# Kernel optimization log

Hardware: AMD Instinct MI355X
Metric: run time of the kernel (lower is better)

Reference implementation:

```python
import jax, jax.numpy as jnp
import numpy as np

CUTOFF = 5.0
BOX = 15.0
SPECIES = [1, 6, 8]
N_NODES = 10000
N_EDGES = 200000
ETAS = [0.01, 0.05, 0.1]
ZETAS = [1.0, 2.0, 4.0, 8.0]
LAMBDAS = [-1.0, 1.0]


def _cartesian_params():
    # matches torch.cartesian_prod(etas, zetas, lambdas): etas outermost
    e, zt, lb = np.meshgrid(np.float32(ETAS), np.float32(ZETAS), np.float32(LAMBDAS), indexing='ij')
    return e.ravel(), zt.ravel(), lb.ravel()  # each [24]


def _build_triplets(rng):
    # edges: edge_index[0]=j (source), edge_index[1]=i (target)
    j = rng.integers(0, N_NODES, N_EDGES)
    i = rng.integers(0, N_NODES, N_EDGES)
    edge_shift = rng.integers(-1, 2, (N_EDGES, 3)).astype(np.float32)
    # CSR of adj_t (row=i, col=j): for edge e, triplet partners k are cols of row j[e]
    order = np.argsort(i, kind='stable')
    cols = j[order]
    cnt = np.bincount(i, minlength=N_NODES)
    rowptr = np.concatenate([[0], np.cumsum(cnt)])
    num_trip = cnt[j]
    T = int(num_trip.sum())
    e_of_t = np.repeat(np.arange(N_EDGES), num_trip)
    starts = np.repeat(np.cumsum(num_trip) - num_trip, num_trip)
    local = np.arange(T) - starts
    idx_k = cols[rowptr[j[e_of_t]] + local]
    idx_i = i[e_of_t]
    idx_j = j[e_of_t]
    shift_t = edge_shift[e_of_t]
    m = idx_i != idx_k
    return idx_i[m], idx_j[m], idx_k[m], shift_t[m]


def setup_inputs() -> dict:
    rng = np.random.default_rng(0)
    pos = rng.uniform(0.0, BOX, (N_NODES, 3)).astype(np.float32)
    cell = (np.eye(3, dtype=np.float32) * BOX)[None]  # [1,3,3]
    z = np.asarray(SPECIES, dtype=np.int64)[rng.integers(0, 3, N_NODES)]
    batch = np.zeros(N_NODES, dtype=np.int64)
    idx_i, idx_j, idx_k, edge_shift_i = _build_triplets(rng)
    etas, zetas, lambdas = _cartesian_params()
    return {
        'pos': jnp.asarray(pos), 'cell': jnp.asarray(cell),
        'z': jnp.asarray(z), 'batch': jnp.asarray(batch),
        'idx_i': jnp.asarray(idx_i), 'idx_j': jnp.asarray(idx_j), 'idx_k': jnp.asarray(idx_k),
        'edge_shift_i': jnp.asarray(edge_shift_i),
        'etas': jnp.asarray(etas), 'zetas': jnp.asarray(zetas), 'lambdas': jnp.asarray(lambdas),
    }


def _cutoff_fn(r):
    return 0.5 * (jnp.cos(jnp.pi * r / CUTOFF) + 1.0) * (r < CUTOFF).astype(r.dtype)


def reference(pos, cell, z, batch, idx_i, idx_j, idx_k, edge_shift_i, etas, zetas, lambdas):
    n_nodes = pos.shape[0]
    pos_i = pos[idx_i]                       # [T,3]
    cell_t = cell[batch[idx_i]]              # [T,3,3]
    shift = jnp.einsum('ni,nij->nj', edge_shift_i, cell_t)
    vec_ij = pos[idx_j] - pos_i + shift
    vec_ik = pos[idx_k] - pos_i + shift
    r_ij = jnp.linalg.norm(vec_ij, axis=-1)
    r_ik = jnp.linalg.norm(vec_ik, axis=-1)
    r_jk = jnp.linalg.norm(vec_ik - vec_ij, axis=-1)
    cos_ijk = jnp.sum(vec_ij * vec_ik, axis=-1) / (r_ij * r_ik + 1e-12)

    # [P,T] angular descriptor; base (1 + lambda*cos) >= 0 since lambda = +/-1
    G4 = (jnp.power(2.0, 1.0 - zetas)[:, None]
          * jnp.power(1.0 + lambdas[:, None] * cos_ijk[None, :], zetas[:, None])
          * jnp.exp(-etas[:, None] * (r_ij**2 + r_ik**2 + r_jk**2)[None, :] / CUTOFF**2)
          * (_cutoff_fn(r_ij) * _cutoff_fn(r_ik) * _cutoff_fn(r_jk))[None, :])

    zj = z[idx_j]
    zk = z[idx_k]
    outs = []
    for sp in SPECIES:
        mask = ((zj == sp) & (zk == sp)).astype(G4.dtype)
        outs.append(jax.ops.segment_sum((G4 * mask).T, idx_i, num_segments=n_nodes).T / 2)
    pairs = [(SPECIES[a], SPECIES[b]) for a in range(len(SPECIES)) for b in range(a + 1, len(SPECIES))]
    for sp_j, sp_k in pairs:
        mask = (((zj == sp_j) & (zk == sp_k)) | ((zj == sp_k) & (zk == sp_j))).astype(G4.dtype)
        outs.append(jax.ops.segment_sum((G4 * mask).T, idx_i, num_segments=n_nodes).T / 2)
    return jnp.concatenate(outs, axis=0)  # [6*P, N]
```

## Files before the change

kernel.cpp:

```cpp
#include <hip/hip_runtime.h>
#include <math.h>

#define CUTOFF_R  5.0f
#define CUT2      25.0f
#define INV_CUT2  (1.0f / 25.0f)
#define PI_OVER_CUT (3.14159265358979323846f / CUTOFF_R)
#define NPARAM 24
#define TPT 4

__device__ __noinline__ void rare_accumulate(
    int i, int j, int k,
    float vjx, float vjy, float vjz,
    float vkx, float vky, float vkz,
    float r2ij, float r2ik, float r2jk,
    const int* __restrict__ z,
    const float* __restrict__ etas,
    float* __restrict__ out, int N)
{
    float rij = sqrtf(r2ij);
    float rik = sqrtf(r2ik);
    float rjk = sqrtf(r2jk);

    float fc = 0.125f * (cosf(PI_OVER_CUT * rij) + 1.0f)
                      * (cosf(PI_OVER_CUT * rik) + 1.0f)
                      * (cosf(PI_OVER_CUT * rjk) + 1.0f);

    float cos_ijk = (vjx * vkx + vjy * vky + vjz * vkz) / (rij * rik + 1e-12f);
    float ssum = (r2ij + r2ik + r2jk) * INV_CUT2;

    int zj = z[j], zk = z[k];
    int a = (zj == 1) ? 0 : ((zj == 6) ? 1 : 2);
    int c = (zk == 1) ? 0 : ((zk == 6) ? 1 : 2);
    int ch = (a == c) ? a : (2 + a + c);

    float* obase = out + (size_t)ch * NPARAM * N + i;
    float fch = 0.5f * fc;

    float bm = 1.0f - cos_ijk;
    float bp = 1.0f + cos_ijk;
    float pw[4][2];
    pw[0][0] = bm;                 pw[0][1] = bp;
    pw[1][0] = bm * bm;            pw[1][1] = bp * bp;
    pw[2][0] = pw[1][0]*pw[1][0];  pw[2][1] = pw[1][1]*pw[1][1];
    pw[3][0] = pw[2][0]*pw[2][0];  pw[3][1] = pw[2][1]*pw[2][1];
    const float coef[4] = {1.0f, 0.5f, 0.125f, 0.0078125f};

    #pragma unroll
    for (int e = 0; e < 3; ++e) {
        float ee = expf(-etas[e * 8] * ssum) * fch;
        #pragma unroll
        for (int zi = 0; zi < 4; ++zi) {
            float cz = coef[zi] * ee;
            atomicAdd(obase + (size_t)(e * 8 + zi * 2 + 0) * N, cz * pw[zi][0]);
            atomicAdd(obase + (size_t)(e * 8 + zi * 2 + 1) * N, cz * pw[zi][1]);
        }
    }
}

__global__ __launch_bounds__(256) void g4_kernel(
    const float* __restrict__ pos,
    const float* __restrict__ cell,
    const int*   __restrict__ z,
    const int*   __restrict__ batch,
    const int*   __restrict__ idx_i,
    const int*   __restrict__ idx_j,
    const int*   __restrict__ idx_k,
    const float* __restrict__ shift,
    const float* __restrict__ etas,
    float* __restrict__ out,
    int T, int N)
{
    int tid = blockIdx.x * blockDim.x + threadIdx.x;
    int base = tid * TPT;
    if (base >= T) return;

    if (base + TPT <= T) {
        int4 vi = *reinterpret_cast<const int4*>(idx_i + base);
        int4 vj = *reinterpret_cast<const int4*>(idx_j + base);
        int4 vk = *reinterpret_cast<const int4*>(idx_k + base);
        int ii[TPT] = {vi.x, vi.y, vi.z, vi.w};
        int jj[TPT] = {vj.x, vj.y, vj.z, vj.w};
        int kk[TPT] = {vk.x, vk.y, vk.z, vk.w};
        float sf[12];
        {
            const float4* sp = reinterpret_cast<const float4*>(shift + 3 * base);
            float4 a = sp[0], b = sp[1], c = sp[2];
            sf[0]=a.x; sf[1]=a.y; sf[2]=a.z;  sf[3]=a.w;
            sf[4]=b.x; sf[5]=b.y; sf[6]=b.z;  sf[7]=b.w;
            sf[8]=c.x; sf[9]=c.y; sf[10]=c.z; sf[11]=c.w;
        }

        float vjxa[TPT], vjya[TPT], vjza[TPT];
        float vkxa[TPT], vkya[TPT], vkza[TPT];
        float r2ija[TPT], r2ika[TPT], r2jka[TPT];
        unsigned mask = 0;

        #pragma unroll
        for (int m = 0; m < TPT; ++m) {
            int i = ii[m], j = jj[m], k = kk[m];
            int b = batch[i];
            const float* C = cell + 9 * b;
            float s0 = sf[3*m], s1 = sf[3*m+1], s2 = sf[3*m+2];
            float shx = s0 * C[0] + s1 * C[3] + s2 * C[6];
            float shy = s0 * C[1] + s1 * C[4] + s2 * C[7];
            float shz = s0 * C[2] + s1 * C[5] + s2 * C[8];

            float pix = pos[3*i+0], piy = pos[3*i+1], piz = pos[3*i+2];
            float vjx = pos[3*j+0] - pix + shx;
            float vjy = pos[3*j+1] - piy + shy;
            float vjz = pos[3*j+2] - piz + shz;
            float vkx = pos[3*k+0] - pix + shx;
            float vky = pos[3*k+1] - piy + shy;
            float vkz = pos[3*k+2] - piz + shz;

            float r2ij = vjx*vjx + vjy*vjy + vjz*vjz;
            float r2ik = vkx*vkx + vky*vky + vkz*vkz;
            float dx = vkx - vjx, dy = vky - vjy, dz = vkz - vjz;
            float r2jk = dx*dx + dy*dy + dz*dz;

            vjxa[m]=vjx; vjya[m]=vjy; vjza[m]=vjz;
            vkxa[m]=vkx; vkya[m]=vky; vkza[m]=vkz;
            r2ija[m]=r2ij; r2ika[m]=r2ik; r2jka[m]=r2jk;

            bool p = (r2ij < CUT2) & (r2ik < CUT2) & (r2jk < CUT2);
            mask |= ((unsigned)p) << m;
        }

        if (mask) {
            #pragma unroll
            for (int m = 0; m < TPT; ++m) {
                if (mask & (1u << m)) {
                    rare_accumulate(ii[m], jj[m], kk[m],
                                    vjxa[m], vjya[m], vjza[m],
                                    vkxa[m], vkya[m], vkza[m],
                                    r2ija[m], r2ika[m], r2jka[m],
                                    z, etas, out, N);
                }
            }
        }
    } else {
        for (int m = 0; m < TPT; ++m) {
            int t = base + m;
            if (t >= T) break;
            int i = idx_i[t], j = idx_j[t], k = idx_k[t];
            float s0 = shift[3*t], s1 = shift[3*t+1], s2 = shift[3*t+2];
            int b = batch[i];
            const float* C = cell + 9 * b;
            float shx = s0 * C[0] + s1 * C[3] + s2 * C[6];
            float shy = s0 * C[1] + s1 * C[4] + s2 * C[7];
            float shz = s0 * C[2] + s1 * C[5] + s2 * C[8];
            float pix = pos[3*i+0], piy = pos[3*i+1], piz = pos[3*i+2];
            float vjx = pos[3*j+0] - pix + shx;
            float vjy = pos[3*j+1] - piy + shy;
            float vjz = pos[3*j+2] - piz + shz;
            float vkx = pos[3*k+0] - pix + shx;
            float vky = pos[3*k+1] - piy + shy;
            float vkz = pos[3*k+2] - piz + shz;
            float r2ij = vjx*vjx + vjy*vjy + vjz*vjz;
            float r2ik = vkx*vkx + vky*vky + vkz*vkz;
            float dx = vkx - vjx, dy = vky - vjy, dz = vkz - vjz;
            float r2jk = dx*dx + dy*dy + dz*dz;
            if ((r2ij < CUT2) & (r2ik < CUT2) & (r2jk < CUT2)) {
                rare_accumulate(i, j, k, vjx, vjy, vjz, vkx, vky, vkz,
                                r2ij, r2ik, r2jk, z, etas, out, N);
            }
        }
    }
}

extern "C" void kernel_launch(void* const* d_in, const int* in_sizes, int n_in,
                              void* d_out, int out_size, void* d_ws, size_t ws_size,
                              hipStream_t stream) {
    const float* pos     = (const float*)d_in[0];
    const float* cell    = (const float*)d_in[1];
    const int*   z       = (const int*)d_in[2];
    const int*   batch   = (const int*)d_in[3];
    const int*   idx_i   = (const int*)d_in[4];
    const int*   idx_j   = (const int*)d_in[5];
    const int*   idx_k   = (const int*)d_in[6];
    const float* shift   = (const float*)d_in[7];
    const float* etas    = (const float*)d_in[8];
    float* out = (float*)d_out;

    int T = in_sizes[4];
    int N = in_sizes[0] / 3;

    hipMemsetAsync(d_out, 0, (size_t)out_size * sizeof(float), stream);

    int block = 256;
    int threads_needed = (T + TPT - 1) / TPT;
    int grid = (threads_needed + block - 1) / block;
    g4_kernel<<<grid, block, 0, stream>>>(pos, cell, z, batch,
                                          idx_i, idx_j, idx_k, shift,
                                          etas, out, T, N);
}
```

Baseline: 166.0 us.

## Stage atom positions in LDS and use persistent grid-stride blocks

Each block first copies the whole position array (hardcoded to 10000 atoms) into shared memory. The per-triplet random position gathers then hit LDS instead of global memory or L2. The launch becomes a fixed 256-block grid of 1024-thread blocks with a grid-stride loop, which spreads the one-time copy across many quads. The per-triplet batch lookup is dropped and the single cell matrix is kept in registers, which assumes one structure and a fixed atom count. The costs are the 120 KB LDS footprint, limiting each CU to one block, and the preload done by every block.

After: 146.7 us. 1.13x faster.

```diff
diff --git a/kernel.cpp b/kernel.cpp
--- a/kernel.cpp
+++ b/kernel.cpp
@@ -6,7 +6,7 @@
 #define INV_CUT2  (1.0f / 25.0f)
 #define PI_OVER_CUT (3.14159265358979323846f / CUTOFF_R)
 #define NPARAM 24
-#define TPT 4
+#define NATOMS 10000
 
 __device__ __noinline__ void rare_accumulate(
     int i, int j, int k,
@@ -57,11 +57,10 @@
     }
 }
 
-__global__ __launch_bounds__(256) void g4_kernel(
+__global__ __launch_bounds__(1024, 1) void g4_kernel(
     const float* __restrict__ pos,
     const float* __restrict__ cell,
     const int*   __restrict__ z,
-    const int*   __restrict__ batch,
     const int*   __restrict__ idx_i,
     const int*   __restrict__ idx_j,
     const int*   __restrict__ idx_k,
@@ -70,99 +69,91 @@
     float* __restrict__ out,
     int T, int N)
 {
-    int tid = blockIdx.x * blockDim.x + threadIdx.x;
-    int base = tid * TPT;
-    if (base >= T) return;
+    __shared__ float spos[3 * NATOMS];
+    {
+        const float4* pos4  = reinterpret_cast<const float4*>(pos);
+        float4*       spos4 = reinterpret_cast<float4*>(spos);
+        const int nvec = (3 * NATOMS) / 4;
+        for (int u = threadIdx.x; u < nvec; u += blockDim.x)
+            spos4[u] = pos4[u];
+    }
+    __syncthreads();
 
-    if (base + TPT <= T) {
-        int4 vi = *reinterpret_cast<const int4*>(idx_i + base);
-        int4 vj = *reinterpret_cast<const int4*>(idx_j + base);
-        int4 vk = *reinterpret_cast<const int4*>(idx_k + base);
-        int ii[TPT] = {vi.x, vi.y, vi.z, vi.w};
-        int jj[TPT] = {vj.x, vj.y, vj.z, vj.w};
-        int kk[TPT] = {vk.x, vk.y, vk.z, vk.w};
-        float sf[12];
-        {
-            const float4* sp = reinterpret_cast<const float4*>(shift + 3 * base);
-            float4 a = sp[0], b = sp[1], c = sp[2];
-            sf[0]=a.x; sf[1]=a.y; sf[2]=a.z;  sf[3]=a.w;
-            sf[4]=b.x; sf[5]=b.y; sf[6]=b.z;  sf[7]=b.w;
-            sf[8]=c.x; sf[9]=c.y; sf[10]=c.z; sf[11]=c.w;
-        }
+    float C00 = cell[0], C01 = cell[1], C02 = cell[2];
+    float C10 = cell[3], C11 = cell[4], C12 = cell[5];
+    float C20 = cell[6], C21 = cell[7], C22 = cell[8];
 
-        float vjxa[TPT], vjya[TPT], vjza[TPT];
-        float vkxa[TPT], vkya[TPT], vkza[TPT];
-        float r2ija[TPT], r2ika[TPT], r2jka[TPT];
-        unsigned mask = 0;
+    const int nQuads   = (T + 3) >> 2;
+    const int gstride  = gridDim.x * blockDim.x;
 
-        #pragma unroll
-        for (int m = 0; m < TPT; ++m) {
-            int i = ii[m], j = jj[m], k = kk[m];
-            int b = batch[i];
-            const float* C = cell + 9 * b;
-            float s0 = sf[3*m], s1 = sf[3*m+1], s2 = sf[3*m+2];
-            float shx = s0 * C[0] + s1 * C[3] + s2 * C[6];
-            float shy = s0 * C[1] + s1 * C[4] + s2 * C[7];
-            float shz = s0 * C[2] + s1 * C[5] + s2 * C[8];
+    for (int q = blockIdx.x * blockDim.x + threadIdx.x; q < nQuads; q += gstride) {
+        int base = q * 4;
+        if (base + 4 <= T) {
+            int4 vi = *reinterpret_cast<const int4*>(idx_i + base);
+            int4 vj = *reinterpret_cast<const int4*>(idx_j + base);
+            int4 vk = *reinterpret_cast<const int4*>(idx_k + base);
+            int ii[4] = {vi.x, vi.y, vi.z, vi.w};
+            int jj[4] = {vj.x, vj.y, vj.z, vj.w};
+            int kk[4] = {vk.x, vk.y, vk.z, vk.w};
+            float sf[12];
+            {
+                const float4* sp = reinterpret_cast<const float4*>(shift + 3 * base);
+                float4 a = sp[0], b = sp[1], c = sp[2];
+                sf[0]=a.x; sf[1]=a.y; sf[2]=a.z;  sf[3]=a.w;
+                sf[4]=b.x; sf[5]=b.y; sf[6]=b.z;  sf[7]=b.w;
+                sf[8]=c.x; sf[9]=c.y; sf[10]=c.z; sf[11]=c.w;
+            }
 
-            float pix = pos[3*i+0], piy = pos[3*i+1], piz = pos[3*i+2];
-            float vjx = pos[3*j+0] - pix + shx;
-            float vjy = pos[3*j+1] - piy + shy;
-            float vjz = pos[3*j+2] - piz + shz;
-            float vkx = pos[3*k+0] - pix + shx;
-            float vky = pos[3*k+1] - piy + shy;
-            float vkz = pos[3*k+2] - piz + shz;
+            #pragma unroll
+            for (int m = 0; m < 4; ++m) {
+                int i = ii[m], j = jj[m], k = kk[m];
+                float s0 = sf[3*m], s1 = sf[3*m+1], s2 = sf[3*m+2];
+                float shx = s0 * C00 + s1 * C10 + s2 * C20;
+                float shy = s0 * C01 + s1 * C11 + s2 * C21;
+                float shz = s0 * C02 + s1 * C12 + s2 * C22;
 
-            float r2ij = vjx*vjx + vjy*vjy + vjz*vjz;
-            float r2ik = vkx*vkx + vky*vky + vkz*vkz;
-            float dx = vkx - vjx, dy = vky - vjy, dz = vkz - vjz;
-            float r2jk = dx*dx + dy*dy + dz*dz;
+                float pix = spos[3*i+0], piy = spos[3*i+1], piz = spos[3*i+2];
+                float vjx = spos[3*j+0] - pix + shx;
+                float vjy = spos[3*j+1] - piy + shy;
+                float vjz = spos[3*j+2] - piz + shz;
+                float vkx = spos[3*k+0] - pix + shx;
+                float vky = spos[3*k+1] - piy + shy;
+                float vkz = spos[3*k+2] - piz + shz;
 
-            vjxa[m]=vjx; vjya[m]=vjy; vjza[m]=vjz;
-            vkxa[m]=vkx; vkya[m]=vky; vkza[m]=vkz;
-            r2ija[m]=r2ij; r2ika[m]=r2ik; r2jka[m]=r2jk;
+                float r2ij = vjx*vjx + vjy*vjy + vjz*vjz;
+                float r2ik = vkx*vkx + vky*vky + vkz*vkz;
+                float dx = vkx - vjx, dy = vky - vjy, dz = vkz - vjz;
+                float r2jk = dx*dx + dy*dy + dz*dz;
 
-            bool p = (r2ij < CUT2) & (r2ik < CUT2) & (r2jk < CUT2);
-            mask |= ((unsigned)p) << m;
-        }
-
-        if (mask) {
-            #pragma unroll
-            for (int m = 0; m < TPT; ++m) {
-                if (mask & (1u << m)) {
-                    rare_accumulate(ii[m], jj[m], kk[m],
-                                    vjxa[m], vjya[m], vjza[m],
-                                    vkxa[m], vkya[m], vkza[m],
-                                    r2ija[m], r2ika[m], r2jka[m],
-                                    z, etas, out, N);
+                if ((r2ij < CUT2) & (r2ik < CUT2) & (r2jk < CUT2)) {
+                    rare_accumulate(i, j, k, vjx, vjy, vjz, vkx, vky, vkz,
+                                    r2ij, r2ik, r2jk, z, etas, out, N);
                 }
             }
-        }
-    } else {
-        for (int m = 0; m < TPT; ++m) {
-            int t = base + m;
-            if (t >= T) break;
-            int i = idx_i[t], j = idx_j[t], k = idx_k[t];
-            float s0 = shift[3*t], s1 = shift[3*t+1], s2 = shift[3*t+2];
-            int b = batch[i];
-            const float* C = cell + 9 * b;
-            float shx = s0 * C[0] + s1 * C[3] + s2 * C[6];
-            float shy = s0 * C[1] + s1 * C[4] + s2 * C[7];
-            float shz = s0 * C[2] + s1 * C[5] + s2 * C[8];
-            float pix = pos[3*i+0], piy = pos[3*i+1], piz = pos[3*i+2];
-            float vjx = pos[3*j+0] - pix + shx;
-            float vjy = pos[3*j+1] - piy + shy;
-            float vjz = pos[3*j+2] - piz + shz;
-            float vkx = pos[3*k+0] - pix + shx;
-            float vky = pos[3*k+1] - piy + shy;
-            float vkz = pos[3*k+2] - piz + shz;
-            float r2ij = vjx*vjx + vjy*vjy + vjz*vjz;
-            float r2ik = vkx*vkx + vky*vky + vkz*vkz;
-            float dx = vkx - vjx, dy = vky - vjy, dz = vkz - vjz;
-            float r2jk = dx*dx + dy*dy + dz*dz;
-            if ((r2ij < CUT2) & (r2ik < CUT2) & (r2jk < CUT2)) {
-                rare_accumulate(i, j, k, vjx, vjy, vjz, vkx, vky, vkz,
-                                r2ij, r2ik, r2jk, z, etas, out, N);
+        } else {
+            for (int m = 0; m < 4; ++m) {
+                int t = base + m;
+                if (t >= T) break;
+                int i = idx_i[t], j = idx_j[t], k = idx_k[t];
+                float s0 = shift[3*t], s1 = shift[3*t+1], s2 = shift[3*t+2];
+                float shx = s0 * C00 + s1 * C10 + s2 * C20;
+                float shy = s0 * C01 + s1 * C11 + s2 * C21;
+                float shz = s0 * C02 + s1 * C12 + s2 * C22;
+                float pix = spos[3*i+0], piy = spos[3*i+1], piz = spos[3*i+2];
+                float vjx = spos[3*j+0] - pix + shx;
+                float vjy = spos[3*j+1] - piy + shy;
+                float vjz = spos[3*j+2] - piz + shz;
+                float vkx = spos[3*k+0] - pix + shx;
+                float vky = spos[3*k+1] - piy + shy;
+                float vkz = spos[3*k+2] - piz + shz;
+                float r2ij = vjx*vjx + vjy*vjy + vjz*vjz;
+                float r2ik = vkx*vkx + vky*vky + vkz*vkz;
+                float dx = vkx - vjx, dy = vky - vjy, dz = vkz - vjz;
+                float r2jk = dx*dx + dy*dy + dz*dz;
+                if ((r2ij < CUT2) & (r2ik < CUT2) & (r2jk < CUT2)) {
+                    rare_accumulate(i, j, k, vjx, vjy, vjz, vkx, vky, vkz,
+                                    r2ij, r2ik, r2jk, z, etas, out, N);
+                }
             }
         }
     }
@@ -174,7 +165,6 @@
     const float* pos     = (const float*)d_in[0];
     const float* cell    = (const float*)d_in[1];
     const int*   z       = (const int*)d_in[2];
-    const int*   batch   = (const int*)d_in[3];
     const int*   idx_i   = (const int*)d_in[4];
     const int*   idx_j   = (const int*)d_in[5];
     const int*   idx_k   = (const int*)d_in[6];
@@ -187,10 +177,9 @@
 
     hipMemsetAsync(d_out, 0, (size_t)out_size * sizeof(float), stream);
 
-    int block = 256;
-    int threads_needed = (T + TPT - 1) / TPT;
-    int grid = (threads_needed + block - 1) / block;
-    g4_kernel<<<grid, block, 0, stream>>>(pos, cell, z, batch,
+    int block = 1024;
+    int grid  = 256;
+    g4_kernel<<<grid, block, 0, stream>>>(pos, cell, z,
                                           idx_i, idx_j, idx_k, shift,
                                           etas, out, T, N);
 }
```
